# Kernel tuning notes

Hardware: AMD Instinct MI355X
Metric: run time of the kernel (lower is better)

The kernel has to match this reference:

```python
import jax, jax.numpy as jnp
import numpy as np

N = 100000      # nodes == in_ch (transductive: x = arange(N))
E = 3200000     # nonzeros of sparse hypergraph adjacency G (COO)
D = 128         # i_emb
DROPOUT = 0.1


def setup_inputs() -> dict:
    key = jax.random.key(0)
    k1, k2, k3, k4, k5 = jax.random.split(key, 5)
    x = jnp.arange(N, dtype=jnp.int64) if jax.config.jax_enable_x64 else jnp.arange(N, dtype=jnp.int32)
    row = jax.random.randint(k1, (E,), 0, N, dtype=jnp.int32)
    col = jax.random.randint(k2, (E,), 0, N, dtype=jnp.int32)
    vals = jax.random.uniform(k3, (E,), dtype=jnp.float32)
    # xavier-uniform embedding: bound = sqrt(6/(N+D))
    eb = float(np.sqrt(6.0 / (N + D)))
    embed_w = jax.random.uniform(k4, (N, D), jnp.float32, -eb, eb)
    fb = float(np.sqrt(6.0 / (D + D)))
    fc_w = jax.random.uniform(k5, (D, D), jnp.float32, -fb, fb)
    fc_b = jnp.zeros((D,), jnp.float32)
    return {"x": x, "row": row, "col": col, "vals": vals,
            "embed_w": embed_w, "fc_w": fc_w, "fc_b": fc_b}


def reference(x, row, col, vals, embed_w, fc_w, fc_b):
    e = embed_w[x]                                   # [N, D] embedding lookup
    # SpMM: out[i] = sum_{nz} vals * e[col]  scattered to row
    agg = jax.ops.segment_sum(vals[:, None] * e[col], row, num_segments=e.shape[0])
    m1 = agg + e                                     # residual
    keep = 1.0 - DROPOUT                             # F.dropout (training=True default)
    mask = jax.random.bernoulli(jax.random.key(42), keep, m1.shape)
    m1 = jnp.where(mask, m1 / keep, 0.0)
    x1 = jax.nn.leaky_relu(m1 @ fc_w.T + fc_b, negative_slope=0.2)
    return jnp.concatenate((e, x1), axis=1)          # [N, 2D]
```

## Files before the change

### kernel.cpp

```cpp
#include <hip/hip_runtime.h>


#define NN 100000
#define DD 128
#define EE 3200000
#define SCAN_B 256
#define NBLK ((NN + SCAN_B - 1) / SCAN_B)

__device__ __forceinline__ unsigned rotl32(unsigned v, int s) {
    return (v << s) | (v >> (32 - s));
}

__device__ __forceinline__ bool keep_elem(unsigned idx) {
    unsigned x0 = 0u, x1 = idx;
    const unsigned k0 = 0u, k1 = 42u;
    const unsigned k2 = 0x1BD11BDAu ^ k0 ^ k1;
    x0 += k0; x1 += k1;
#define TFROUND(s) x0 += x1; x1 = rotl32(x1, s); x1 ^= x0;
    TFROUND(13) TFROUND(15) TFROUND(26) TFROUND(6)
    x0 += k1; x1 += k2 + 1u;
    TFROUND(17) TFROUND(29) TFROUND(16) TFROUND(24)
    x0 += k2; x1 += k0 + 2u;
    TFROUND(13) TFROUND(15) TFROUND(26) TFROUND(6)
    x0 += k0; x1 += k1 + 3u;
    TFROUND(17) TFROUND(29) TFROUND(16) TFROUND(24)
    x0 += k1; x1 += k2 + 4u;
    TFROUND(13) TFROUND(15) TFROUND(26) TFROUND(6)
    x0 += k2; x1 += k0 + 5u;
#undef TFROUND
    unsigned bits = x0 ^ x1;
    float u = __uint_as_float((bits >> 9) | 0x3f800000u) - 1.0f;
    return u < 0.9f;
}

__global__ __launch_bounds__(256) void setup_kernel(const float4* __restrict__ emb4,
                                                    uint2* __restrict__ ebf2,
                                                    int4* __restrict__ counts4) {
    int i = blockIdx.x * 256 + threadIdx.x;
    float4 v = emb4[i];
    unsigned a = __float_as_uint(v.x), b = __float_as_uint(v.y);
    unsigned c = __float_as_uint(v.z), d = __float_as_uint(v.w);
    a = (a + 0x7fffu + ((a >> 16) & 1u)) >> 16;
    b = (b + 0x7fffu + ((b >> 16) & 1u)) >> 16;
    c = (c + 0x7fffu + ((c >> 16) & 1u)) >> 16;
    d = (d + 0x7fffu + ((d >> 16) & 1u)) >> 16;
    uint2 o;
    o.x = a | (b << 16);
    o.y = c | (d << 16);
    ebf2[i] = o;
    if (i < NN / 4) counts4[i] = make_int4(0, 0, 0, 0);
}

__global__ __launch_bounds__(256) void hist_kernel(const int4* __restrict__ row4,
                                                   int* __restrict__ counts,
                                                   int4* __restrict__ rank4) {
    int i = blockIdx.x * 256 + threadIdx.x;
    int4 r = row4[i];
    int4 k;
    k.x = atomicAdd(&counts[r.x], 1);
    k.y = atomicAdd(&counts[r.y], 1);
    k.z = atomicAdd(&counts[r.z], 1);
    k.w = atomicAdd(&counts[r.w], 1);
    rank4[i] = k;
}

__global__ __launch_bounds__(SCAN_B) void scan1_kernel(const int* __restrict__ counts,
                                                       int* __restrict__ rowptr,
                                                       int* __restrict__ bsums) {
    __shared__ int s[SCAN_B];
    int t = threadIdx.x;
    int i = blockIdx.x * SCAN_B + t;
    int v = (i < NN) ? counts[i] : 0;
    s[t] = v;
    __syncthreads();
    for (int d = 1; d < SCAN_B; d <<= 1) {
        int a = (t >= d) ? s[t - d] : 0;
        __syncthreads();
        s[t] += a;
        __syncthreads();
    }
    if (i < NN) rowptr[i + 1] = s[t];
    if (t == SCAN_B - 1) bsums[blockIdx.x] = s[t];
}

__global__ __launch_bounds__(512) void scan2_kernel(int* __restrict__ bsums) {
    __shared__ int s[512];
    int t = threadIdx.x;
    int v = (t < NBLK) ? bsums[t] : 0;
    s[t] = v;
    __syncthreads();
    for (int d = 1; d < 512; d <<= 1) {
        int a = (t >= d) ? s[t - d] : 0;
        __syncthreads();
        s[t] += a;
        __syncthreads();
    }
    if (t < NBLK) bsums[t] = s[t] - v;
}

__global__ __launch_bounds__(SCAN_B) void scan3_kernel(int* __restrict__ rowptr,
                                                       const int* __restrict__ bsums) {
    int i = blockIdx.x * SCAN_B + threadIdx.x;
    if (i < NN) rowptr[i + 1] += bsums[i >> 8];
    if (i == 0) rowptr[0] = 0;
}

__device__ __forceinline__ unsigned pack_entry(int xc, float v) {
    unsigned pb = __float_as_uint(v) + 0x10000u;
    return (pb & 0xFFFE0000u) | (unsigned)xc;
}

__global__ __launch_bounds__(256) void fill_kernel(const int* __restrict__ x,
                                                   const int4* __restrict__ row4,
                                                   const int4* __restrict__ col4,
                                                   const float4* __restrict__ vals4,
                                                   const int4* __restrict__ rank4,
                                                   const int* __restrict__ rowptr,
                                                   unsigned* __restrict__ csr) {
    int i = blockIdx.x * 256 + threadIdx.x;
    int4 r = row4[i];
    int4 c = col4[i];
    float4 v = vals4[i];
    int4 k = rank4[i];
    csr[rowptr[r.x] + k.x] = pack_entry(x[c.x], v.x);
    csr[rowptr[r.y] + k.y] = pack_entry(x[c.y], v.y);
    csr[rowptr[r.z] + k.z] = pack_entry(x[c.z], v.z);
    csr[rowptr[r.w] + k.w] = pack_entry(x[c.w], v.w);
}

__global__ __launch_bounds__(256) void gather_kernel(const int* __restrict__ x,
                                                     const int* __restrict__ rowptr,
                                                     const unsigned* __restrict__ csr,
                                                     const unsigned* __restrict__ ebf,
                                                     const float2* __restrict__ emb2,
                                                     float2* __restrict__ out2) {
    int wave = threadIdx.x >> 6;
    int lane = threadIdx.x & 63;
    int n = blockIdx.x * 4 + wave;
    int s = rowptr[n], e = rowptr[n + 1];
    float ax = 0.f, ay = 0.f;
    int j = s;
    for (; j + 4 <= e; j += 4) {
        unsigned p0 = csr[j], p1 = csr[j + 1], p2 = csr[j + 2], p3 = csr[j + 3];
        unsigned b0 = ebf[(long)(p0 & 0x1FFFFu) * 64 + lane];
        unsigned b1 = ebf[(long)(p1 & 0x1FFFFu) * 64 + lane];
        unsigned b2 = ebf[(long)(p2 & 0x1FFFFu) * 64 + lane];
        unsigned b3 = ebf[(long)(p3 & 0x1FFFFu) * 64 + lane];
        float v0 = __uint_as_float(p0 & 0xFFFE0000u);
        float v1 = __uint_as_float(p1 & 0xFFFE0000u);
        float v2 = __uint_as_float(p2 & 0xFFFE0000u);
        float v3 = __uint_as_float(p3 & 0xFFFE0000u);
        ax += v0 * __uint_as_float(b0 << 16) + v1 * __uint_as_float(b1 << 16)
            + v2 * __uint_as_float(b2 << 16) + v3 * __uint_as_float(b3 << 16);
        ay += v0 * __uint_as_float(b0 & 0xffff0000u) + v1 * __uint_as_float(b1 & 0xffff0000u)
            + v2 * __uint_as_float(b2 & 0xffff0000u) + v3 * __uint_as_float(b3 & 0xffff0000u);
    }
    for (; j < e; ++j) {
        unsigned p = csr[j];
        unsigned b = ebf[(long)(p & 0x1FFFFu) * 64 + lane];
        float v = __uint_as_float(p & 0xFFFE0000u);
        ax += v * __uint_as_float(b << 16);
        ay += v * __uint_as_float(b & 0xffff0000u);
    }
    float2 es = emb2[(long)x[n] * 64 + lane];
    out2[(long)n * 128 + lane] = es;
    float2 m1;
    m1.x = ax + es.x;
    m1.y = ay + es.y;
    unsigned base = (unsigned)n * 128u + 2u * (unsigned)lane;
    m1.x = keep_elem(base) ? m1.x * (1.0f / 0.9f) : 0.0f;
    m1.y = keep_elem(base + 1u) ? m1.y * (1.0f / 0.9f) : 0.0f;
    out2[(long)n * 128 + 64 + lane] = m1;
}

__global__ __launch_bounds__(256, 3) void fc3_kernel(float* __restrict__ out,
                                                     const float* __restrict__ fc_w,
                                                     const float* __restrict__ fc_b) {
    __shared__ float ms_t[128][66];
    __shared__ float wc[32][132];
    int tid = threadIdx.x;
    int row0 = blockIdx.x * 64;
    const float4* fcw4 = (const float4*)fc_w;
    const float4* out4c = (const float4*)out;

    for (int chunk = tid; chunk < 64 * 32; chunk += 256) {
        int nl = chunk >> 5;
        int q = chunk & 31;
        int n = row0 + nl;
        float4 v = (n < NN) ? out4c[(long)n * 64 + 32 + q]
                            : make_float4(0.f, 0.f, 0.f, 0.f);
        ms_t[q * 4 + 0][nl] = v.x;
        ms_t[q * 4 + 1][nl] = v.y;
        ms_t[q * 4 + 2][nl] = v.z;
        ms_t[q * 4 + 3][nl] = v.w;
    }

    int cg = tid & 31;
    int rg = tid >> 5;
    float acc[8][4];
#pragma unroll
    for (int r = 0; r < 8; ++r)
#pragma unroll
        for (int c = 0; c < 4; ++c) acc[r][c] = 0.f;

    for (int ch = 0; ch < 4; ++ch) {
        __syncthreads();
        for (int chunk = tid; chunk < 128 * 8; chunk += 256) {
            int jj = chunk >> 3;
            int kq = chunk & 7;
            float4 v = fcw4[jj * 32 + ch * 8 + kq];
            wc[kq * 4 + 0][jj] = v.x;
            wc[kq * 4 + 1][jj] = v.y;
            wc[kq * 4 + 2][jj] = v.z;
            wc[kq * 4 + 3][jj] = v.w;
        }
        __syncthreads();
        int kbase = ch * 32;
#pragma unroll
        for (int kk = 0; kk < 32; ++kk) {
            float4 w4 = *(const float4*)(&wc[kk][cg * 4]);
            int k = kbase + kk;
            float2 m01 = *(const float2*)(&ms_t[k][rg * 8 + 0]);
            float2 m23 = *(const float2*)(&ms_t[k][rg * 8 + 2]);
            float2 m45 = *(const float2*)(&ms_t[k][rg * 8 + 4]);
            float2 m67 = *(const float2*)(&ms_t[k][rg * 8 + 6]);
            float m[8] = {m01.x, m01.y, m23.x, m23.y, m45.x, m45.y, m67.x, m67.y};
#pragma unroll
            for (int r = 0; r < 8; ++r) {
                acc[r][0] += m[r] * w4.x;
                acc[r][1] += m[r] * w4.y;
                acc[r][2] += m[r] * w4.z;
                acc[r][3] += m[r] * w4.w;
            }
        }
    }

    float4 b4 = *(const float4*)(fc_b + cg * 4);
#pragma unroll
    for (int r = 0; r < 8; ++r) {
        int n = row0 + rg * 8 + r;
        if (n >= NN) break;
        float4 o;
        o.x = acc[r][0] + b4.x;
        o.y = acc[r][1] + b4.y;
        o.z = acc[r][2] + b4.z;
        o.w = acc[r][3] + b4.w;
        o.x = o.x >= 0.f ? o.x : 0.2f * o.x;
        o.y = o.y >= 0.f ? o.y : 0.2f * o.y;
        o.z = o.z >= 0.f ? o.z : 0.2f * o.z;
        o.w = o.w >= 0.f ? o.w : 0.2f * o.w;
        *(float4*)(out + (long)n * 256 + 128 + cg * 4) = o;
    }
}

__global__ __launch_bounds__(256) void init_kernel(const int* __restrict__ x,
                                                   const float4* __restrict__ emb4,
                                                   float4* __restrict__ out4) {
    int i = blockIdx.x * 256 + threadIdx.x;
    int n = i >> 5;
    int q = i & 31;
    if (n >= NN) return;
    float4 v = emb4[(long)x[n] * 32 + q];
    out4[(long)n * 64 + q] = v;
    out4[(long)n * 64 + 32 + q] = v;
}

#define EDGES_PER_GROUP 8
__global__ __launch_bounds__(256) void scatter_kernel(const int* __restrict__ x,
                                                      const int* __restrict__ row,
                                                      const int* __restrict__ col,
                                                      const float* __restrict__ vals,
                                                      const float4* __restrict__ emb4,
                                                      float* __restrict__ out) {
    long gid = (long)blockIdx.x * 256 + threadIdx.x;
    long group = gid >> 5;
    int lane = (int)(gid & 31);
    long e0 = group * EDGES_PER_GROUP;
#pragma unroll
    for (int k = 0; k < EDGES_PER_GROUP; ++k) {
        long e = e0 + k;
        if (e >= EE) break;
        int r = row[e];
        int c = col[e];
        float v = vals[e];
        float4 ev = emb4[(long)x[c] * 32 + lane];
        float* dst = out + (long)r * 256 + 128 + lane * 4;
        atomicAdd(dst + 0, v * ev.x);
        atomicAdd(dst + 1, v * ev.y);
        atomicAdd(dst + 2, v * ev.z);
        atomicAdd(dst + 3, v * ev.w);
    }
}

__global__ __launch_bounds__(256) void fc_kernel(float* __restrict__ out,
                                                 const float* __restrict__ fc_w,
                                                 const float* __restrict__ fc_b) {
    __shared__ float wt[128][132];
    __shared__ float ms[32][128];
    int tid = threadIdx.x;
    int row0 = blockIdx.x * 32;

    for (int i = tid; i < 128 * 128; i += 256) {
        int j = i >> 7, k = i & 127;
        wt[k][j] = fc_w[i];
    }
    for (int i = tid; i < 32 * 32; i += 256) {
        int r = i >> 5, q = i & 31;
        long n = row0 + r;
        float4 v = *(const float4*)(out + n * 256 + 128 + q * 4);
        unsigned base = (unsigned)n * 128u + (unsigned)(q * 4);
        float* vp = reinterpret_cast<float*>(&v);
#pragma unroll
        for (int c = 0; c < 4; ++c)
            vp[c] = keep_elem(base + c) ? vp[c] * (1.0f / 0.9f) : 0.0f;
        *(float4*)(&ms[r][q * 4]) = v;
    }
    __syncthreads();

    int rg = tid >> 5;
    int cg = tid & 31;
    float acc[4][4] = {{0.f}};
    for (int k = 0; k < 128; ++k) {
        float4 w4 = *(const float4*)(&wt[k][cg * 4]);
#pragma unroll
        for (int r = 0; r < 4; ++r) {
            float m = ms[rg * 4 + r][k];
            acc[r][0] += m * w4.x;
            acc[r][1] += m * w4.y;
            acc[r][2] += m * w4.z;
            acc[r][3] += m * w4.w;
        }
    }

    float4 b4 = *(const float4*)(fc_b + cg * 4);
#pragma unroll
    for (int r = 0; r < 4; ++r) {
        long n = row0 + rg * 4 + r;
        float4 o;
        o.x = acc[r][0] + b4.x;
        o.y = acc[r][1] + b4.y;
        o.z = acc[r][2] + b4.z;
        o.w = acc[r][3] + b4.w;
        o.x = o.x >= 0.f ? o.x : 0.2f * o.x;
        o.y = o.y >= 0.f ? o.y : 0.2f * o.y;
        o.z = o.z >= 0.f ? o.z : 0.2f * o.z;
        o.w = o.w >= 0.f ? o.w : 0.2f * o.w;
        *(float4*)(out + n * 256 + 128 + cg * 4) = o;
    }
}

extern "C" void kernel_launch(void* const* d_in, const int* in_sizes, int n_in,
                              void* d_out, int out_size, void* d_ws, size_t ws_size,
                              hipStream_t stream) {
    const int*   x    = (const int*)d_in[0];
    const int*   row  = (const int*)d_in[1];
    const int*   col  = (const int*)d_in[2];
    const float* vals = (const float*)d_in[3];
    const float* emb  = (const float*)d_in[4];
    const float* fc_w = (const float*)d_in[5];
    const float* fc_b = (const float*)d_in[6];
    float* out = (float*)d_out;

    size_t off = 0;
    char* ws = (char*)d_ws;
    int* counts = (int*)(ws + off); off += (((size_t)NN * 4) + 255) & ~(size_t)255;
    int* rowptr = (int*)(ws + off); off += (((size_t)(NN + 1) * 4) + 255) & ~(size_t)255;
    int* bsums  = (int*)(ws + off); off += 4096;
    unsigned* csr = (unsigned*)(ws + off); off += (size_t)EE * 4;
    int* rank   = (int*)(ws + off); off += (size_t)EE * 4;
    unsigned* ebf = (unsigned*)(ws + off); off += (size_t)NN * DD * 2;
    size_t need = off;

    if (ws_size >= need) {
        setup_kernel<<<(int)(((long)NN * DD / 4 + 255) / 256), 256, 0, stream>>>(
            (const float4*)emb, (uint2*)ebf, (int4*)counts);
        hist_kernel<<<EE / 4 / 256, 256, 0, stream>>>((const int4*)row, counts, (int4*)rank);
        scan1_kernel<<<NBLK, SCAN_B, 0, stream>>>(counts, rowptr, bsums);
        scan2_kernel<<<1, 512, 0, stream>>>(bsums);
        scan3_kernel<<<NBLK, SCAN_B, 0, stream>>>(rowptr, bsums);
        fill_kernel<<<EE / 4 / 256, 256, 0, stream>>>(x, (const int4*)row, (const int4*)col,
                                                      (const float4*)vals, (const int4*)rank,
                                                      rowptr, csr);
        gather_kernel<<<NN / 4, 256, 0, stream>>>(x, rowptr, csr, ebf,
                                                  (const float2*)emb, (float2*)out);
        fc3_kernel<<<(NN + 63) / 64, 256, 0, stream>>>(out, fc_w, fc_b);
    } else {
        init_kernel<<<(NN * 32 + 255) / 256, 256, 0, stream>>>(x, (const float4*)emb, (float4*)out);
        int scatter_blocks = (int)(((long)EE / EDGES_PER_GROUP) * 32 / 256);
        scatter_kernel<<<scatter_blocks, 256, 0, stream>>>(x, row, col, vals,
                                                           (const float4*)emb, out);
        fc_kernel<<<NN / 32, 256, 0, stream>>>(out, fc_w, fc_b);
    }
}
```

Before: 590.8 us.

## Split per-row histogram counters into sub-buckets and pack ranks into bytes

```diff
diff --git a/kernel.cpp b/kernel.cpp
--- a/kernel.cpp
+++ b/kernel.cpp
@@ -4,8 +4,9 @@
 #define NN 100000
 #define DD 128
 #define EE 3200000
-#define SCAN_B 256
-#define NBLK ((NN + SCAN_B - 1) / SCAN_B)
+#define NSUB (NN * 8)
+#define S1B 1024
+#define NBLK1 ((NSUB + S1B - 1) / S1B)
 
 __device__ __forceinline__ unsigned rotl32(unsigned v, int s) {
     return (v << s) | (v >> (32 - s));
@@ -48,61 +49,61 @@
     o.x = a | (b << 16);
     o.y = c | (d << 16);
     ebf2[i] = o;
-    if (i < NN / 4) counts4[i] = make_int4(0, 0, 0, 0);
+    if (i < NSUB / 4) counts4[i] = make_int4(0, 0, 0, 0);
 }
 
 __global__ __launch_bounds__(256) void hist_kernel(const int4* __restrict__ row4,
                                                    int* __restrict__ counts,
-                                                   int4* __restrict__ rank4) {
+                                                   unsigned* __restrict__ rank4) {
     int i = blockIdx.x * 256 + threadIdx.x;
     int4 r = row4[i];
-    int4 k;
-    k.x = atomicAdd(&counts[r.x], 1);
-    k.y = atomicAdd(&counts[r.y], 1);
-    k.z = atomicAdd(&counts[r.z], 1);
-    k.w = atomicAdd(&counts[r.w], 1);
-    rank4[i] = k;
-}
-
-__global__ __launch_bounds__(SCAN_B) void scan1_kernel(const int* __restrict__ counts,
-                                                       int* __restrict__ rowptr,
-                                                       int* __restrict__ bsums) {
-    __shared__ int s[SCAN_B];
+    int sb = (i & 1) << 2;
+    unsigned k0 = (unsigned)atomicAdd(&counts[r.x * 8 + sb + 0], 1);
+    unsigned k1 = (unsigned)atomicAdd(&counts[r.y * 8 + sb + 1], 1);
+    unsigned k2 = (unsigned)atomicAdd(&counts[r.z * 8 + sb + 2], 1);
+    unsigned k3 = (unsigned)atomicAdd(&counts[r.w * 8 + sb + 3], 1);
+    rank4[i] = k0 | (k1 << 8) | (k2 << 16) | (k3 << 24);
+}
+
+__global__ __launch_bounds__(S1B) void scan1_kernel(const int* __restrict__ counts,
+                                                    int* __restrict__ subptr,
+                                                    int* __restrict__ bsums) {
+    __shared__ int s[S1B];
     int t = threadIdx.x;
-    int i = blockIdx.x * SCAN_B + t;
-    int v = (i < NN) ? counts[i] : 0;
+    int i = blockIdx.x * S1B + t;
+    int v = (i < NSUB) ? counts[i] : 0;
     s[t] = v;
     __syncthreads();
-    for (int d = 1; d < SCAN_B; d <<= 1) {
+    for (int d = 1; d < S1B; d <<= 1) {
         int a = (t >= d) ? s[t - d] : 0;
         __syncthreads();
         s[t] += a;
         __syncthreads();
     }
-    if (i < NN) rowptr[i + 1] = s[t];
-    if (t == SCAN_B - 1) bsums[blockIdx.x] = s[t];
-}
-
-__global__ __launch_bounds__(512) void scan2_kernel(int* __restrict__ bsums) {
-    __shared__ int s[512];
+    if (i < NSUB) subptr[i + 1] = s[t];
+    if (t == S1B - 1) bsums[blockIdx.x] = s[t];
+}
+
+__global__ __launch_bounds__(S1B) void scan2_kernel(int* __restrict__ bsums) {
+    __shared__ int s[S1B];
     int t = threadIdx.x;
-    int v = (t < NBLK) ? bsums[t] : 0;
+    int v = (t < NBLK1) ? bsums[t] : 0;
     s[t] = v;
     __syncthreads();
-    for (int d = 1; d < 512; d <<= 1) {
+    for (int d = 1; d < S1B; d <<= 1) {
         int a = (t >= d) ? s[t - d] : 0;
         __syncthreads();
         s[t] += a;
         __syncthreads();
     }
-    if (t < NBLK) bsums[t] = s[t] - v;
-}
-
-__global__ __launch_bounds__(SCAN_B) void scan3_kernel(int* __restrict__ rowptr,
-                                                       const int* __restrict__ bsums) {
-    int i = blockIdx.x * SCAN_B + threadIdx.x;
-    if (i < NN) rowptr[i + 1] += bsums[i >> 8];
-    if (i == 0) rowptr[0] = 0;
+    if (t < NBLK1) bsums[t] = s[t] - v;
+}
+
+__global__ __launch_bounds__(S1B) void scan3_kernel(int* __restrict__ subptr,
+                                                    const int* __restrict__ bsums) {
+    int i = blockIdx.x * S1B + threadIdx.x;
+    if (i < NSUB) subptr[i + 1] += bsums[i >> 10];
+    if (i == 0) subptr[0] = 0;
 }
 
 __device__ __forceinline__ unsigned pack_entry(int xc, float v) {
@@ -114,22 +115,23 @@
                                                    const int4* __restrict__ row4,
                                                    const int4* __restrict__ col4,
                                                    const float4* __restrict__ vals4,
-                                                   const int4* __restrict__ rank4,
-                                                   const int* __restrict__ rowptr,
+                                                   const unsigned* __restrict__ rank4,
+                                                   const int* __restrict__ subptr,
                                                    unsigned* __restrict__ csr) {
     int i = blockIdx.x * 256 + threadIdx.x;
     int4 r = row4[i];
     int4 c = col4[i];
     float4 v = vals4[i];
-    int4 k = rank4[i];
-    csr[rowptr[r.x] + k.x] = pack_entry(x[c.x], v.x);
-    csr[rowptr[r.y] + k.y] = pack_entry(x[c.y], v.y);
-    csr[rowptr[r.z] + k.z] = pack_entry(x[c.z], v.z);
-    csr[rowptr[r.w] + k.w] = pack_entry(x[c.w], v.w);
+    unsigned kk = rank4[i];
+    int sb = (i & 1) << 2;
+    csr[subptr[r.x * 8 + sb + 0] + (kk & 0xffu)]         = pack_entry(x[c.x], v.x);
+    csr[subptr[r.y * 8 + sb + 1] + ((kk >> 8) & 0xffu)]  = pack_entry(x[c.y], v.y);
+    csr[subptr[r.z * 8 + sb + 2] + ((kk >> 16) & 0xffu)] = pack_entry(x[c.z], v.z);
+    csr[subptr[r.w * 8 + sb + 3] + (kk >> 24)]           = pack_entry(x[c.w], v.w);
 }
 
 __global__ __launch_bounds__(256) void gather_kernel(const int* __restrict__ x,
-                                                     const int* __restrict__ rowptr,
+                                                     const int* __restrict__ subptr,
                                                      const unsigned* __restrict__ csr,
                                                      const unsigned* __restrict__ ebf,
                                                      const float2* __restrict__ emb2,
@@ -137,7 +139,7 @@
     int wave = threadIdx.x >> 6;
     int lane = threadIdx.x & 63;
     int n = blockIdx.x * 4 + wave;
-    int s = rowptr[n], e = rowptr[n + 1];
+    int s = subptr[n * 8], e = subptr[n * 8 + 8];
     float ax = 0.f, ay = 0.f;
     int j = s;
     for (; j + 4 <= e; j += 4) {
@@ -363,25 +365,24 @@
 
     size_t off = 0;
     char* ws = (char*)d_ws;
-    int* counts = (int*)(ws + off); off += (((size_t)NN * 4) + 255) & ~(size_t)255;
-    int* rowptr = (int*)(ws + off); off += (((size_t)(NN + 1) * 4) + 255) & ~(size_t)255;
+    int* counts = (int*)(ws + off); off += (size_t)NSUB * 4;
+    int* subptr = (int*)(ws + off); off += (((size_t)(NSUB + 1) * 4) + 255) & ~(size_t)255;
     int* bsums  = (int*)(ws + off); off += 4096;
     unsigned* csr = (unsigned*)(ws + off); off += (size_t)EE * 4;
-    int* rank   = (int*)(ws + off); off += (size_t)EE * 4;
+    unsigned* rank = (unsigned*)(ws + off); off += (size_t)EE;
     unsigned* ebf = (unsigned*)(ws + off); off += (size_t)NN * DD * 2;
     size_t need = off;
 
     if (ws_size >= need) {
         setup_kernel<<<(int)(((long)NN * DD / 4 + 255) / 256), 256, 0, stream>>>(
             (const float4*)emb, (uint2*)ebf, (int4*)counts);
-        hist_kernel<<<EE / 4 / 256, 256, 0, stream>>>((const int4*)row, counts, (int4*)rank);
-        scan1_kernel<<<NBLK, SCAN_B, 0, stream>>>(counts, rowptr, bsums);
-        scan2_kernel<<<1, 512, 0, stream>>>(bsums);
-        scan3_kernel<<<NBLK, SCAN_B, 0, stream>>>(rowptr, bsums);
+        hist_kernel<<<EE / 4 / 256, 256, 0, stream>>>((const int4*)row, counts, rank);
+        scan1_kernel<<<NBLK1, S1B, 0, stream>>>(counts, subptr, bsums);
+        scan2_kernel<<<1, S1B, 0, stream>>>(bsums);
+        scan3_kernel<<<NBLK1, S1B, 0, stream>>>(subptr, bsums);
         fill_kernel<<<EE / 4 / 256, 256, 0, stream>>>(x, (const int4*)row, (const int4*)col,
-                                                      (const float4*)vals, (const int4*)rank,
-                                                      rowptr, csr);
-        gather_kernel<<<NN / 4, 256, 0, stream>>>(x, rowptr, csr, ebf,
+                                                      (const float4*)vals, rank, subptr, csr);
+        gather_kernel<<<NN / 4, 256, 0, stream>>>(x, subptr, csr, ebf,
                                                   (const float2*)emb, (float2*)out);
         fc3_kernel<<<(NN + 63) / 64, 256, 0, stream>>>(out, fc_w, fc_b);
     } else {
```

After: 599.9 us. No clear change (+1.5%).
